# Optimization experiments

Measured on AMD Instinct MI355X. Metric: run time of the kernel, lower is better.

The kernel has to match this reference:

```python
import jax, jax.numpy as jnp
import numpy as np

T, H, I, E, SI, TOP_K = 1024, 2048, 1408, 60, 5632, 4


def setup_inputs() -> dict:
    key = jax.random.key(0)
    ks = jax.random.split(key, 9)
    s = 0.02  # typical init scale for weights
    return {
        "x": jax.random.normal(ks[0], (T, H), jnp.float32),
        "router_w": jax.random.normal(ks[1], (E, H), jnp.float32) * s,
        "w_gate": jax.random.normal(ks[2], (E, I, H), jnp.float32) * s,
        "w_up": jax.random.normal(ks[3], (E, I, H), jnp.float32) * s,
        "w_down": jax.random.normal(ks[4], (E, H, I), jnp.float32) * s,
        "sw_gate": jax.random.normal(ks[5], (SI, H), jnp.float32) * s,
        "sw_up": jax.random.normal(ks[6], (SI, H), jnp.float32) * s,
        "sw_down": jax.random.normal(ks[7], (H, SI), jnp.float32) * s,
        "shared_gate_w": jax.random.normal(ks[8], (1, H), jnp.float32) * s,
        "top_k": TOP_K,
    }


def reference(x, router_w, w_gate, w_up, w_down, sw_gate, sw_up, sw_down, shared_gate_w, top_k):
    Ttok, Hdim = x.shape
    Eexp = router_w.shape[0]
    # --- router: softmax over experts, top-k selection (norm_topk_prob=False) ---
    logits = x @ router_w.T                          # [T,E]
    probs = jax.nn.softmax(logits, axis=-1)
    topk_p, topk_i = jax.lax.top_k(probs, top_k)     # [T,k]
    # dense combine weights: zero for unrouted experts
    combine = jnp.zeros((Ttok, Eexp), x.dtype)
    combine = combine.at[jnp.arange(Ttok)[:, None], topk_i].set(topk_p)  # [T,E]

    # --- routed experts: SwiGLU MLP per expert, weighted accumulate (scan over E) ---
    def expert_step(acc, w):
        wg, wu, wd, c = w                            # [I,H],[I,H],[H,I],[T]
        h = jax.nn.silu(x @ wg.T) * (x @ wu.T)       # [T,I]
        return acc + c[:, None] * (h @ wd.T), None

    moe_out, _ = jax.lax.scan(expert_step, jnp.zeros_like(x),
                              (w_gate, w_up, w_down, combine.T))

    # --- shared expert with sigmoid gate ---
    shared = (jax.nn.silu(x @ sw_gate.T) * (x @ sw_up.T)) @ sw_down.T    # [T,H]
    shared = jax.nn.sigmoid(x @ shared_gate_w.T) * shared                # [T,1]*[T,H]
    return moe_out + shared
```

## Files before the change

### kernel.cpp

```cpp
#include <hip/hip_runtime.h>
#include <hip/hip_bf16.h>


typedef float  f32x4  __attribute__((ext_vector_type(4)));
typedef short  bf16x8 __attribute__((ext_vector_type(8)));
typedef unsigned short u16;
typedef unsigned int   u32;

constexpr int TT = 1024, HD = 2048, ID = 1408, NE = 60, SID = 5632, KTOP = 4;

#define GLDS(g, l) __builtin_amdgcn_global_load_lds( \
    (const __attribute__((address_space(1))) void*)(g), \
    (__attribute__((address_space(3))) void*)(l), 16, 0, 0)

__device__ __forceinline__ u16 f2bf(float f) {
    union { float f; u32 u; } v; v.f = f;
    u32 r = v.u + 0x7FFFu + ((v.u >> 16) & 1u);
    return (u16)(r >> 16);
}
__device__ __forceinline__ u32 cvtpk(float a, float b) {
    u32 r; asm("v_cvt_pk_bf16_f32 %0, %1, %2" : "=v"(r) : "v"(a), "v"(b));
    return r;
}
__device__ __forceinline__ bf16x8 fragF32(const float* tile, int r, int lk) {
    const float4* p = (const float4*)(tile + r * 32 + (((lk << 1) ^ ((r & 3) << 1)) << 2));
    float4 a = p[0], b = p[1];
    union { u32 u[4]; bf16x8 v; } rr;
    rr.u[0] = cvtpk(a.x, a.y); rr.u[1] = cvtpk(a.z, a.w);
    rr.u[2] = cvtpk(b.x, b.y); rr.u[3] = cvtpk(b.z, b.w);
    return rr.v;
}
__device__ __forceinline__ bf16x8 fragB16(const u16* tile, int r, int lk) {
    return *(const bf16x8*)(tile + r * 32 + ((lk ^ (r & 3)) << 3));
}

__global__ __launch_bounds__(64) void router_k(
    const float* __restrict__ x, const float* __restrict__ rw,
    const float* __restrict__ sgw,
    float* __restrict__ topk_p, int* __restrict__ topk_i,
    int* __restrict__ cnt, float* __restrict__ sgate)
{
    const int t = blockIdx.x, l = threadIdx.x;
    const float4* xr = ((const float4*)(x + (size_t)t * HD)) + l * 8;
    float4 xa[8];
    #pragma unroll
    for (int i = 0; i < 8; i++) xa[i] = xr[i];

    float le = 0.f;
    for (int e = 0; e < NE; e++) {
        const float4* wr = ((const float4*)(rw + (size_t)e * HD)) + l * 8;
        float a = 0.f;
        #pragma unroll
        for (int i = 0; i < 8; i++) {
            float4 wv = wr[i];
            a += xa[i].x * wv.x + xa[i].y * wv.y + xa[i].z * wv.z + xa[i].w * wv.w;
        }
        #pragma unroll
        for (int s = 32; s; s >>= 1) a += __shfl_xor(a, s);
        if (l == e) le = a;
    }
    {
        const float4* wr = ((const float4*)sgw) + l * 8;
        float a = 0.f;
        #pragma unroll
        for (int i = 0; i < 8; i++) {
            float4 wv = wr[i];
            a += xa[i].x * wv.x + xa[i].y * wv.y + xa[i].z * wv.z + xa[i].w * wv.w;
        }
        #pragma unroll
        for (int s = 32; s; s >>= 1) a += __shfl_xor(a, s);
        if (l == 0) sgate[t] = 1.f / (1.f + __expf(-a));
    }
    float mv = (l < NE) ? le : -3.4e38f;
    #pragma unroll
    for (int s = 32; s; s >>= 1) mv = fmaxf(mv, __shfl_xor(mv, s));
    float p = (l < NE) ? __expf(le - mv) : 0.f;
    float ss = p;
    #pragma unroll
    for (int s = 32; s; s >>= 1) ss += __shfl_xor(ss, s);
    p /= ss;
    float pv = (l < NE) ? p : -1.f;
    int   pi = l;
    float kp = 0.f; int ki = 0;
    for (int k = 0; k < KTOP; k++) {
        float bv = pv; int bi = pi;
        #pragma unroll
        for (int s = 32; s; s >>= 1) {
            float ov = __shfl_xor(bv, s); int oi = __shfl_xor(bi, s);
            if (ov > bv || (ov == bv && oi < bi)) { bv = ov; bi = oi; }
        }
        if (l == k) { kp = bv; ki = bi; }
        if (pi == bi) pv = -1.f;
    }
    if (l < KTOP) {
        topk_p[t * KTOP + l] = kp;
        topk_i[t * KTOP + l] = ki;
        atomicAdd(&cnt[ki], 1);
    }
}

__global__ __launch_bounds__(64) void prefix_k(const int* __restrict__ cnt, int* __restrict__ base)
{
    int l = threadIdx.x;
    if (l < NE) {
        int s = 0;
        for (int j = 0; j < l; j++) s += cnt[j];
        base[l] = s;
    }
}

__global__ __launch_bounds__(256) void scatter_k(
    const float* __restrict__ topk_p, const int* __restrict__ topk_i,
    const int* __restrict__ base, int* __restrict__ fill,
    int* __restrict__ slot_tok, float* __restrict__ slot_wt)
{
    int t = blockIdx.x * blockDim.x + threadIdx.x;
    if (t >= TT) return;
    for (int k = 0; k < KTOP; k++) {
        int e = topk_i[t * KTOP + k];
        int pos = atomicAdd(&fill[e], 1);
        int s = base[e] + pos;
        slot_tok[s] = t;
        slot_wt[s]  = topk_p[t * KTOP + k];
    }
}

template<bool GROUPED>
__global__ __launch_bounds__(256, 2) void gu_k(
    const float* __restrict__ X,
    const float* __restrict__ Wg, const float* __restrict__ Wu, size_t bStride,
    u16* __restrict__ H,
    const int* __restrict__ slot_tok, const float* __restrict__ slot_wt,
    const int* __restrict__ cnt, const int* __restrict__ basearr,
    int K, int N)
{
    __shared__ float Asl[2][128 * 32];
    __shared__ float Bgsl[2][64 * 32];
    __shared__ float Busl[2][64 * 32];
    const int tid = threadIdx.x, w = tid >> 6, lane = tid & 63;
    const int lm = lane & 15, lk = lane >> 4, wm0 = w * 32;
    const int e = GROUPED ? blockIdx.z : 0;
    const int mcnt = GROUPED ? cnt[e] : 128;
    const int mbase = GROUPED ? basearr[e] : blockIdx.y * 128;
    const float* Bg = Wg + (size_t)e * bStride + (size_t)blockIdx.x * 64 * K;
    const float* Bu = Wu + (size_t)e * bStride + (size_t)blockIdx.x * 64 * K;
    const int aofs = ((lane & 7) ^ (((lane >> 3) & 3) << 1)) << 2;
    const float* bgrow[2]; const float* burow[2];
    #pragma unroll
    for (int j = 0; j < 2; j++) {
        int rB = w * 16 + j * 8 + (lane >> 3);
        bgrow[j] = Bg + (size_t)rB * K + aofs;
        burow[j] = Bu + (size_t)rB * K + aofs;
    }
    const int nk = K >> 5;

    for (int mt = 0; GROUPED ? (mt * 128 < mcnt) : (mt == 0); ++mt) {
        const float* arow[4];
        #pragma unroll
        for (int j = 0; j < 4; j++) {
            int rA = w * 32 + j * 8 + (lane >> 3);
            int row;
            if constexpr (GROUPED) {
                int sl = mbase + mt * 128 + rA;
                row = (mt * 128 + rA < mcnt) ? slot_tok[sl] : 0;
            } else row = mbase + rA;
            arow[j] = X + (size_t)row * K + aofs;
        }
        f32x4 ag[2][4], au[2][4];
        #pragma unroll
        for (int mf = 0; mf < 2; mf++)
            #pragma unroll
            for (int nf = 0; nf < 4; nf++) {
                ag[mf][nf] = f32x4{0.f, 0.f, 0.f, 0.f};
                au[mf][nf] = f32x4{0.f, 0.f, 0.f, 0.f};
            }

        auto stage = [&](int b, int kt) {
            #pragma unroll
            for (int j = 0; j < 4; j++)
                GLDS(arow[j] + kt, &Asl[b][w * 1024 + j * 256]);
            #pragma unroll
            for (int j = 0; j < 2; j++) {
                GLDS(bgrow[j] + kt, &Bgsl[b][w * 512 + j * 256]);
                GLDS(burow[j] + kt, &Busl[b][w * 512 + j * 256]);
            }
        };

        stage(0, 0);
        __syncthreads();
        int cur = 0;
        for (int t = 0; t < nk; ++t) {
            if (t + 1 < nk) stage(cur ^ 1, (t + 1) << 5);
            const float* At  = &Asl[cur][0];
            const float* Bgt = &Bgsl[cur][0];
            const float* But = &Busl[cur][0];
            bf16x8 afr[2];
            #pragma unroll
            for (int mf = 0; mf < 2; mf++) afr[mf] = fragF32(At, wm0 + mf * 16 + lm, lk);
            #pragma unroll
            for (int nf = 0; nf < 4; nf++) {
                bf16x8 bgf = fragF32(Bgt, nf * 16 + lm, lk);
                bf16x8 buf_ = fragF32(But, nf * 16 + lm, lk);
                #pragma unroll
                for (int mf = 0; mf < 2; mf++) {
                    ag[mf][nf] = __builtin_amdgcn_mfma_f32_16x16x32_bf16(afr[mf], bgf, ag[mf][nf], 0, 0, 0);
                    au[mf][nf] = __builtin_amdgcn_mfma_f32_16x16x32_bf16(afr[mf], buf_, au[mf][nf], 0, 0, 0);
                }
            }
            __syncthreads();
            cur ^= 1;
        }

        #pragma unroll
        for (int mf = 0; mf < 2; mf++)
            #pragma unroll
            for (int j = 0; j < 4; j++) {
                int m = wm0 + mf * 16 + lk * 4 + j;
                bool valid = GROUPED ? (mt * 128 + m < mcnt) : true;
                if (valid) {
                    size_t row; float wt;
                    if constexpr (GROUPED) {
                        size_t sl = (size_t)(mbase + mt * 128 + m);
                        row = sl; wt = slot_wt[sl];
                    } else { row = (size_t)(mbase + m); wt = 1.f; }
                    #pragma unroll
                    for (int nf = 0; nf < 4; nf++) {
                        int col = blockIdx.x * 64 + nf * 16 + lm;
                        float g = ag[mf][nf][j], u = au[mf][nf][j];
                        float hv = g / (1.f + __expf(-g)) * u * wt;
                        H[row * (size_t)N + col] = f2bf(hv);
                    }
                }
            }
    }
}

template<bool GROUPED>
__global__ __launch_bounds__(256, 4) void down_k(
    const u16* __restrict__ Hb, const float* __restrict__ W0, size_t bStride,
    float* __restrict__ outF,
    const int* __restrict__ slot_tok, const float* __restrict__ sgate,
    const int* __restrict__ cnt, const int* __restrict__ basearr,
    int K, int kspan, int N)
{
    __shared__ u16   Asl[2][128 * 32];
    __shared__ float Bsl[2][64 * 32];
    const int tid = threadIdx.x, w = tid >> 6, lane = tid & 63;
    const int lm = lane & 15, lk = lane >> 4, wm0 = w * 32;
    const int e = GROUPED ? blockIdx.z : 0;
    const int mcnt = GROUPED ? cnt[e] : 128;
    const int mbase = GROUPED ? basearr[e] : blockIdx.y * 128;
    const int kbeg = GROUPED ? 0 : blockIdx.z * kspan;
    const int nk = (GROUPED ? K : kspan) >> 5;
    const float* Bp = W0 + (size_t)e * bStride + (size_t)blockIdx.x * 64 * K + kbeg;
    const int aofsF = ((lane & 7) ^ (((lane >> 3) & 3) << 1)) << 2;
    const int aofsH = ((lane & 3) ^ ((lane >> 2) & 3)) << 3;
    const float* brow[2];
    #pragma unroll
    for (int j = 0; j < 2; j++) {
        int rB = w * 16 + j * 8 + (lane >> 3);
        brow[j] = Bp + (size_t)rB * K + aofsF;
    }

    for (int mt = 0; GROUPED ? (mt * 128 < mcnt) : (mt == 0); ++mt) {
        const u16* arow[2];
        #pragma unroll
        for (int j = 0; j < 2; j++) {
            int rA = w * 32 + j * 16 + (lane >> 2);
            int row;
            if constexpr (GROUPED) {
                row = (mt * 128 + rA < mcnt) ? (mbase + mt * 128 + rA) : mbase;
            } else row = mbase + rA;
            arow[j] = Hb + (size_t)row * K + kbeg + aofsH;
        }
        f32x4 acc[2][4];
        #pragma unroll
        for (int mf = 0; mf < 2; mf++)
            #pragma unroll
            for (int nf = 0; nf < 4; nf++) acc[mf][nf] = f32x4{0.f, 0.f, 0.f, 0.f};

        auto stage = [&](int b, int kt) {
            #pragma unroll
            for (int j = 0; j < 2; j++)
                GLDS(arow[j] + kt, &Asl[b][w * 1024 + j * 512]);
            #pragma unroll
            for (int j = 0; j < 2; j++)
                GLDS(brow[j] + kt, &Bsl[b][w * 512 + j * 256]);
        };

        stage(0, 0);
        __syncthreads();
        int cur = 0;
        for (int t = 0; t < nk; ++t) {
            if (t + 1 < nk) stage(cur ^ 1, (t + 1) << 5);
            const u16*   At = &Asl[cur][0];
            const float* Bt = &Bsl[cur][0];
            bf16x8 afr[2];
            #pragma unroll
            for (int mf = 0; mf < 2; mf++) afr[mf] = fragB16(At, wm0 + mf * 16 + lm, lk);
            #pragma unroll
            for (int nf = 0; nf < 4; nf++) {
                bf16x8 bfr = fragF32(Bt, nf * 16 + lm, lk);
                #pragma unroll
                for (int mf = 0; mf < 2; mf++)
                    acc[mf][nf] = __builtin_amdgcn_mfma_f32_16x16x32_bf16(afr[mf], bfr, acc[mf][nf], 0, 0, 0);
            }
            __syncthreads();
            cur ^= 1;
        }

        #pragma unroll
        for (int mf = 0; mf < 2; mf++)
            #pragma unroll
            for (int j = 0; j < 4; j++) {
                int m = wm0 + mf * 16 + lk * 4 + j;
                bool valid = GROUPED ? (mt * 128 + m < mcnt) : true;
                if (valid) {
                    int tok; float scale;
                    if constexpr (GROUPED) {
                        tok = slot_tok[mbase + mt * 128 + m]; scale = 1.f;
                    } else { tok = mbase + m; scale = sgate[tok]; }
                    #pragma unroll
                    for (int nf = 0; nf < 4; nf++) {
                        int col = blockIdx.x * 64 + nf * 16 + lm;
                        atomicAdd(&outF[(size_t)tok * N + col], scale * acc[mf][nf][j]);
                    }
                }
            }
    }
}

extern "C" void kernel_launch(void* const* d_in, const int* in_sizes, int n_in,
                              void* d_out, int out_size, void* d_ws, size_t ws_size,
                              hipStream_t stream)
{
    const float* x      = (const float*)d_in[0];
    const float* rw     = (const float*)d_in[1];
    const float* w_gate = (const float*)d_in[2];
    const float* w_up   = (const float*)d_in[3];
    const float* w_down = (const float*)d_in[4];
    const float* sw_g   = (const float*)d_in[5];
    const float* sw_u   = (const float*)d_in[6];
    const float* sw_d   = (const float*)d_in[7];
    const float* sgw    = (const float*)d_in[8];
    float* out = (float*)d_out;

    char* ws = (char*)d_ws;
    int*   cnt      = (int*)(ws + 0);
    int*   fill     = (int*)(ws + 256);
    int*   basea    = (int*)(ws + 512);
    float* sgate    = (float*)(ws + 768);
    float* topk_p   = (float*)(ws + 5120);
    int*   topk_i   = (int*)(ws + 21504);
    int*   slot_tok = (int*)(ws + 37888);
    float* slot_wt  = (float*)(ws + 54272);
    u16*   h  = (u16*)(ws + 71680);
    u16*   hs = h + (size_t)4096 * ID;

    hipMemsetAsync(ws, 0, 512, stream);
    hipMemsetAsync(d_out, 0, (size_t)TT * HD * sizeof(float), stream);

    router_k<<<TT, 64, 0, stream>>>(x, rw, sgw, topk_p, topk_i, cnt, sgate);
    prefix_k<<<1, 64, 0, stream>>>(cnt, basea);
    scatter_k<<<4, 256, 0, stream>>>(topk_p, topk_i, basea, fill, slot_tok, slot_wt);

    gu_k<true><<<dim3(ID / 64, 1, NE), 256, 0, stream>>>(
        x, w_gate, w_up, (size_t)ID * HD, h,
        slot_tok, slot_wt, cnt, basea, HD, ID);
    gu_k<false><<<dim3(SID / 64, TT / 128, 1), 256, 0, stream>>>(
        x, sw_g, sw_u, 0, hs,
        nullptr, nullptr, nullptr, nullptr, HD, SID);
    down_k<true><<<dim3(HD / 64, 1, NE), 256, 0, stream>>>(
        h, w_down, (size_t)HD * ID, out,
        slot_tok, nullptr, cnt, basea, ID, 0, HD);
    down_k<false><<<dim3(HD / 64, TT / 128, 2), 256, 0, stream>>>(
        hs, sw_d, 0, out,
        nullptr, sgate, nullptr, nullptr, SID, SID / 2, HD);
}
```

Baseline: 831.9 us.

## Replace LDS-staged GEMMs with direct register-fragment loads and pre-converted bf16 activations

Drops the LDS double-buffered tiles in the gate/up and down GEMMs. Each wave now loads its MFMA fragments straight from global memory into registers with a two-stage software prefetch, over a 2x2 wave tile of 64x32. A new kernel converts x to bf16 once so activation fragments need no conversion in the inner loop. The shared down-projection now runs first without a K split and writes output directly, which removes the output memset and its atomics, and a small kernel replaces the counter memset. The trade is no LDS reuse across waves: each weight row is fetched by several waves and row reads are uncoalesced, with higher register pressure.

```diff
diff --git a/kernel.cpp b/kernel.cpp
--- a/kernel.cpp
+++ b/kernel.cpp
@@ -9,10 +9,6 @@
 
 constexpr int TT = 1024, HD = 2048, ID = 1408, NE = 60, SID = 5632, KTOP = 4;
 
-#define GLDS(g, l) __builtin_amdgcn_global_load_lds( \
-    (const __attribute__((address_space(1))) void*)(g), \
-    (__attribute__((address_space(3))) void*)(l), 16, 0, 0)
-
 __device__ __forceinline__ u16 f2bf(float f) {
     union { float f; u32 u; } v; v.f = f;
     u32 r = v.u + 0x7FFFu + ((v.u >> 16) & 1u);
@@ -22,16 +18,30 @@
     u32 r; asm("v_cvt_pk_bf16_f32 %0, %1, %2" : "=v"(r) : "v"(a), "v"(b));
     return r;
 }
-__device__ __forceinline__ bf16x8 fragF32(const float* tile, int r, int lk) {
-    const float4* p = (const float4*)(tile + r * 32 + (((lk << 1) ^ ((r & 3) << 1)) << 2));
-    float4 a = p[0], b = p[1];
+__device__ __forceinline__ bf16x8 cvt8(float4 a, float4 b) {
     union { u32 u[4]; bf16x8 v; } rr;
     rr.u[0] = cvtpk(a.x, a.y); rr.u[1] = cvtpk(a.z, a.w);
     rr.u[2] = cvtpk(b.x, b.y); rr.u[3] = cvtpk(b.z, b.w);
     return rr.v;
 }
-__device__ __forceinline__ bf16x8 fragB16(const u16* tile, int r, int lk) {
-    return *(const bf16x8*)(tile + r * 32 + ((lk ^ (r & 3)) << 3));
+__device__ __forceinline__ bf16x8 asbf(uint4 v) {
+    union { uint4 u; bf16x8 b; } c; c.u = v; return c.b;
+}
+
+__global__ void zero_k(int* __restrict__ p) { p[threadIdx.x] = 0; }
+
+__global__ __launch_bounds__(256) void xcvt_k(const float* __restrict__ x, u16* __restrict__ xb)
+{
+    size_t i = ((size_t)blockIdx.x * 256 + threadIdx.x) * 16;
+    const float4* p = (const float4*)(x + i);
+    float4 f0 = p[0], f1 = p[1], f2 = p[2], f3 = p[3];
+    uint4 o0, o1;
+    o0.x = cvtpk(f0.x, f0.y); o0.y = cvtpk(f0.z, f0.w);
+    o0.z = cvtpk(f1.x, f1.y); o0.w = cvtpk(f1.z, f1.w);
+    o1.x = cvtpk(f2.x, f2.y); o1.y = cvtpk(f2.z, f2.w);
+    o1.z = cvtpk(f3.x, f3.y); o1.w = cvtpk(f3.z, f3.w);
+    ((uint4*)(xb + i))[0] = o0;
+    ((uint4*)(xb + i))[1] = o1;
 }
 
 __global__ __launch_bounds__(64) void router_k(
@@ -127,92 +137,85 @@
 
 template<bool GROUPED>
 __global__ __launch_bounds__(256, 2) void gu_k(
-    const float* __restrict__ X,
+    const u16* __restrict__ Xb,
     const float* __restrict__ Wg, const float* __restrict__ Wu, size_t bStride,
     u16* __restrict__ H,
     const int* __restrict__ slot_tok, const float* __restrict__ slot_wt,
     const int* __restrict__ cnt, const int* __restrict__ basearr,
     int K, int N)
 {
-    __shared__ float Asl[2][128 * 32];
-    __shared__ float Bgsl[2][64 * 32];
-    __shared__ float Busl[2][64 * 32];
     const int tid = threadIdx.x, w = tid >> 6, lane = tid & 63;
-    const int lm = lane & 15, lk = lane >> 4, wm0 = w * 32;
+    const int lm = lane & 15, lk = lane >> 4;
+    const int wm0 = (w >> 1) * 64, wn0 = (w & 1) * 32;
     const int e = GROUPED ? blockIdx.z : 0;
     const int mcnt = GROUPED ? cnt[e] : 128;
-    const int mbase = GROUPED ? basearr[e] : blockIdx.y * 128;
-    const float* Bg = Wg + (size_t)e * bStride + (size_t)blockIdx.x * 64 * K;
-    const float* Bu = Wu + (size_t)e * bStride + (size_t)blockIdx.x * 64 * K;
-    const int aofs = ((lane & 7) ^ (((lane >> 3) & 3) << 1)) << 2;
-    const float* bgrow[2]; const float* burow[2];
-    #pragma unroll
-    for (int j = 0; j < 2; j++) {
-        int rB = w * 16 + j * 8 + (lane >> 3);
-        bgrow[j] = Bg + (size_t)rB * K + aofs;
-        burow[j] = Bu + (size_t)rB * K + aofs;
-    }
-    const int nk = K >> 5;
+    const int mbase = GROUPED ? basearr[e] : 0;
+
+    const float* gP[2]; const float* uP[2];
+    #pragma unroll
+    for (int nf = 0; nf < 2; nf++) {
+        size_t row = (size_t)(blockIdx.x * 64 + wn0 + nf * 16 + lm);
+        gP[nf] = Wg + (size_t)e * bStride + row * K + lk * 8;
+        uP[nf] = Wu + (size_t)e * bStride + row * K + lk * 8;
+    }
 
     for (int mt = 0; GROUPED ? (mt * 128 < mcnt) : (mt == 0); ++mt) {
-        const float* arow[4];
-        #pragma unroll
-        for (int j = 0; j < 4; j++) {
-            int rA = w * 32 + j * 8 + (lane >> 3);
+        const u16* aP[4];
+        #pragma unroll
+        for (int mf = 0; mf < 4; mf++) {
+            int mrow = wm0 + mf * 16 + lm;
             int row;
             if constexpr (GROUPED) {
-                int sl = mbase + mt * 128 + rA;
-                row = (mt * 128 + rA < mcnt) ? slot_tok[sl] : 0;
-            } else row = mbase + rA;
-            arow[j] = X + (size_t)row * K + aofs;
-        }
-        f32x4 ag[2][4], au[2][4];
-        #pragma unroll
-        for (int mf = 0; mf < 2; mf++)
+                int sl = mbase + mt * 128 + mrow;
+                row = (mt * 128 + mrow < mcnt) ? slot_tok[sl] : slot_tok[mbase];
+            } else row = blockIdx.y * 128 + mrow;
+            aP[mf] = Xb + (size_t)row * K + lk * 8;
+        }
+
+        f32x4 acc[2][4][2];
+        #pragma unroll
+        for (int m = 0; m < 2; m++)
             #pragma unroll
-            for (int nf = 0; nf < 4; nf++) {
-                ag[mf][nf] = f32x4{0.f, 0.f, 0.f, 0.f};
-                au[mf][nf] = f32x4{0.f, 0.f, 0.f, 0.f};
-            }
-
-        auto stage = [&](int b, int kt) {
-            #pragma unroll
-            for (int j = 0; j < 4; j++)
-                GLDS(arow[j] + kt, &Asl[b][w * 1024 + j * 256]);
-            #pragma unroll
-            for (int j = 0; j < 2; j++) {
-                GLDS(bgrow[j] + kt, &Bgsl[b][w * 512 + j * 256]);
-                GLDS(burow[j] + kt, &Busl[b][w * 512 + j * 256]);
-            }
-        };
-
-        stage(0, 0);
-        __syncthreads();
-        int cur = 0;
-        for (int t = 0; t < nk; ++t) {
-            if (t + 1 < nk) stage(cur ^ 1, (t + 1) << 5);
-            const float* At  = &Asl[cur][0];
-            const float* Bgt = &Bgsl[cur][0];
-            const float* But = &Busl[cur][0];
-            bf16x8 afr[2];
-            #pragma unroll
-            for (int mf = 0; mf < 2; mf++) afr[mf] = fragF32(At, wm0 + mf * 16 + lm, lk);
-            #pragma unroll
-            for (int nf = 0; nf < 4; nf++) {
-                bf16x8 bgf = fragF32(Bgt, nf * 16 + lm, lk);
-                bf16x8 buf_ = fragF32(But, nf * 16 + lm, lk);
+            for (int mf = 0; mf < 4; mf++)
                 #pragma unroll
-                for (int mf = 0; mf < 2; mf++) {
-                    ag[mf][nf] = __builtin_amdgcn_mfma_f32_16x16x32_bf16(afr[mf], bgf, ag[mf][nf], 0, 0, 0);
-                    au[mf][nf] = __builtin_amdgcn_mfma_f32_16x16x32_bf16(afr[mf], buf_, au[mf][nf], 0, 0, 0);
-                }
-            }
-            __syncthreads();
-            cur ^= 1;
-        }
-
-        #pragma unroll
-        for (int mf = 0; mf < 2; mf++)
+                for (int nf = 0; nf < 2; nf++)
+                    acc[m][mf][nf] = f32x4{0.f, 0.f, 0.f, 0.f};
+
+        uint4  a0[4], a1[4];
+        float4 g0[2][2], u0[2][2], g1[2][2], u1[2][2];
+
+#define LOADA(dst, kt) do { _Pragma("unroll") \
+        for (int mf = 0; mf < 4; mf++) dst[mf] = *(const uint4*)(aP[mf] + (kt)); } while (0)
+#define LOADB(dg, du, kt) do { _Pragma("unroll") \
+        for (int nf = 0; nf < 2; nf++) { \
+            const float4* pg = (const float4*)(gP[nf] + (kt)); \
+            dg[nf][0] = pg[0]; dg[nf][1] = pg[1]; \
+            const float4* pu = (const float4*)(uP[nf] + (kt)); \
+            du[nf][0] = pu[0]; du[nf][1] = pu[1]; } } while (0)
+#define COMPUTE(av, gv, uv) do { _Pragma("unroll") \
+        for (int nf = 0; nf < 2; nf++) { \
+            bf16x8 bg = cvt8(gv[nf][0], gv[nf][1]); \
+            bf16x8 bu = cvt8(uv[nf][0], uv[nf][1]); \
+            _Pragma("unroll") \
+            for (int mf = 0; mf < 4; mf++) { \
+                bf16x8 af = asbf(av[mf]); \
+                acc[0][mf][nf] = __builtin_amdgcn_mfma_f32_16x16x32_bf16(af, bg, acc[0][mf][nf], 0, 0, 0); \
+                acc[1][mf][nf] = __builtin_amdgcn_mfma_f32_16x16x32_bf16(af, bu, acc[1][mf][nf], 0, 0, 0); \
+            } } } while (0)
+
+        LOADA(a0, 0); LOADB(g0, u0, 0);
+        for (int kt = 0; kt < K; kt += 64) {
+            LOADA(a1, kt + 32); LOADB(g1, u1, kt + 32);
+            COMPUTE(a0, g0, u0);
+            if (kt + 64 < K) { LOADA(a0, kt + 64); LOADB(g0, u0, kt + 64); }
+            COMPUTE(a1, g1, u1);
+        }
+#undef LOADA
+#undef LOADB
+#undef COMPUTE
+
+        #pragma unroll
+        for (int mf = 0; mf < 4; mf++)
             #pragma unroll
             for (int j = 0; j < 4; j++) {
                 int m = wm0 + mf * 16 + lk * 4 + j;
@@ -222,11 +225,11 @@
                     if constexpr (GROUPED) {
                         size_t sl = (size_t)(mbase + mt * 128 + m);
                         row = sl; wt = slot_wt[sl];
-                    } else { row = (size_t)(mbase + m); wt = 1.f; }
+                    } else { row = (size_t)(blockIdx.y * 128 + m); wt = 1.f; }
                     #pragma unroll
-                    for (int nf = 0; nf < 4; nf++) {
-                        int col = blockIdx.x * 64 + nf * 16 + lm;
-                        float g = ag[mf][nf][j], u = au[mf][nf][j];
+                    for (int nf = 0; nf < 2; nf++) {
+                        int col = blockIdx.x * 64 + wn0 + nf * 16 + lm;
+                        float g = acc[0][mf][nf][j], u = acc[1][mf][nf][j];
                         float hv = g / (1.f + __expf(-g)) * u * wt;
                         H[row * (size_t)N + col] = f2bf(hv);
                     }
@@ -236,94 +239,92 @@
 }
 
 template<bool GROUPED>
-__global__ __launch_bounds__(256, 4) void down_k(
+__global__ __launch_bounds__(256, 3) void down_k(
     const u16* __restrict__ Hb, const float* __restrict__ W0, size_t bStride,
     float* __restrict__ outF,
     const int* __restrict__ slot_tok, const float* __restrict__ sgate,
     const int* __restrict__ cnt, const int* __restrict__ basearr,
-    int K, int kspan, int N)
-{
-    __shared__ u16   Asl[2][128 * 32];
-    __shared__ float Bsl[2][64 * 32];
+    int K, int N)
+{
     const int tid = threadIdx.x, w = tid >> 6, lane = tid & 63;
-    const int lm = lane & 15, lk = lane >> 4, wm0 = w * 32;
+    const int lm = lane & 15, lk = lane >> 4;
+    const int wm0 = (w >> 1) * 64, wn0 = (w & 1) * 32;
     const int e = GROUPED ? blockIdx.z : 0;
     const int mcnt = GROUPED ? cnt[e] : 128;
-    const int mbase = GROUPED ? basearr[e] : blockIdx.y * 128;
-    const int kbeg = GROUPED ? 0 : blockIdx.z * kspan;
-    const int nk = (GROUPED ? K : kspan) >> 5;
-    const float* Bp = W0 + (size_t)e * bStride + (size_t)blockIdx.x * 64 * K + kbeg;
-    const int aofsF = ((lane & 7) ^ (((lane >> 3) & 3) << 1)) << 2;
-    const int aofsH = ((lane & 3) ^ ((lane >> 2) & 3)) << 3;
-    const float* brow[2];
-    #pragma unroll
-    for (int j = 0; j < 2; j++) {
-        int rB = w * 16 + j * 8 + (lane >> 3);
-        brow[j] = Bp + (size_t)rB * K + aofsF;
+    const int mbase = GROUPED ? basearr[e] : 0;
+
+    const float* bP[2];
+    #pragma unroll
+    for (int nf = 0; nf < 2; nf++) {
+        size_t row = (size_t)(blockIdx.x * 64 + wn0 + nf * 16 + lm);
+        bP[nf] = W0 + (size_t)e * bStride + row * K + lk * 8;
     }
 
     for (int mt = 0; GROUPED ? (mt * 128 < mcnt) : (mt == 0); ++mt) {
-        const u16* arow[2];
-        #pragma unroll
-        for (int j = 0; j < 2; j++) {
-            int rA = w * 32 + j * 16 + (lane >> 2);
+        const u16* aP[4];
+        #pragma unroll
+        for (int mf = 0; mf < 4; mf++) {
+            int mrow = wm0 + mf * 16 + lm;
             int row;
             if constexpr (GROUPED) {
-                row = (mt * 128 + rA < mcnt) ? (mbase + mt * 128 + rA) : mbase;
-            } else row = mbase + rA;
-            arow[j] = Hb + (size_t)row * K + kbeg + aofsH;
-        }
-        f32x4 acc[2][4];
-        #pragma unroll
-        for (int mf = 0; mf < 2; mf++)
+                int sl = mbase + mt * 128 + mrow;
+                row = (mt * 128 + mrow < mcnt) ? sl : mbase;
+            } else row = blockIdx.y * 128 + mrow;
+            aP[mf] = Hb + (size_t)row * K + lk * 8;
+        }
+
+        f32x4 acc[4][2];
+        #pragma unroll
+        for (int mf = 0; mf < 4; mf++)
             #pragma unroll
-            for (int nf = 0; nf < 4; nf++) acc[mf][nf] = f32x4{0.f, 0.f, 0.f, 0.f};
-
-        auto stage = [&](int b, int kt) {
-            #pragma unroll
-            for (int j = 0; j < 2; j++)
-                GLDS(arow[j] + kt, &Asl[b][w * 1024 + j * 512]);
-            #pragma unroll
-            for (int j = 0; j < 2; j++)
-                GLDS(brow[j] + kt, &Bsl[b][w * 512 + j * 256]);
-        };
-
-        stage(0, 0);
-        __syncthreads();
-        int cur = 0;
-        for (int t = 0; t < nk; ++t) {
-            if (t + 1 < nk) stage(cur ^ 1, (t + 1) << 5);
-            const u16*   At = &Asl[cur][0];
-            const float* Bt = &Bsl[cur][0];
-            bf16x8 afr[2];
-            #pragma unroll
-            for (int mf = 0; mf < 2; mf++) afr[mf] = fragB16(At, wm0 + mf * 16 + lm, lk);
-            #pragma unroll
-            for (int nf = 0; nf < 4; nf++) {
-                bf16x8 bfr = fragF32(Bt, nf * 16 + lm, lk);
-                #pragma unroll
-                for (int mf = 0; mf < 2; mf++)
-                    acc[mf][nf] = __builtin_amdgcn_mfma_f32_16x16x32_bf16(afr[mf], bfr, acc[mf][nf], 0, 0, 0);
-            }
-            __syncthreads();
-            cur ^= 1;
-        }
-
-        #pragma unroll
-        for (int mf = 0; mf < 2; mf++)
+            for (int nf = 0; nf < 2; nf++)
+                acc[mf][nf] = f32x4{0.f, 0.f, 0.f, 0.f};
+
+        uint4  a0[4], a1[4];
+        float4 b0[2][2], b1[2][2];
+
+#define LOADA(dst, kt) do { _Pragma("unroll") \
+        for (int mf = 0; mf < 4; mf++) dst[mf] = *(const uint4*)(aP[mf] + (kt)); } while (0)
+#define LOADB(db, kt) do { _Pragma("unroll") \
+        for (int nf = 0; nf < 2; nf++) { \
+            const float4* pb = (const float4*)(bP[nf] + (kt)); \
+            db[nf][0] = pb[0]; db[nf][1] = pb[1]; } } while (0)
+#define COMPUTE(av, bv) do { _Pragma("unroll") \
+        for (int nf = 0; nf < 2; nf++) { \
+            bf16x8 bf_ = cvt8(bv[nf][0], bv[nf][1]); \
+            _Pragma("unroll") \
+            for (int mf = 0; mf < 4; mf++) \
+                acc[mf][nf] = __builtin_amdgcn_mfma_f32_16x16x32_bf16(asbf(av[mf]), bf_, acc[mf][nf], 0, 0, 0); \
+        } } while (0)
+
+        LOADA(a0, 0); LOADB(b0, 0);
+        for (int kt = 0; kt < K; kt += 64) {
+            LOADA(a1, kt + 32); LOADB(b1, kt + 32);
+            COMPUTE(a0, b0);
+            if (kt + 64 < K) { LOADA(a0, kt + 64); LOADB(b0, kt + 64); }
+            COMPUTE(a1, b1);
+        }
+#undef LOADA
+#undef LOADB
+#undef COMPUTE
+
+        #pragma unroll
+        for (int mf = 0; mf < 4; mf++)
             #pragma unroll
             for (int j = 0; j < 4; j++) {
                 int m = wm0 + mf * 16 + lk * 4 + j;
                 bool valid = GROUPED ? (mt * 128 + m < mcnt) : true;
                 if (valid) {
-                    int tok; float scale;
-                    if constexpr (GROUPED) {
-                        tok = slot_tok[mbase + mt * 128 + m]; scale = 1.f;
-                    } else { tok = mbase + m; scale = sgate[tok]; }
                     #pragma unroll
-                    for (int nf = 0; nf < 4; nf++) {
-                        int col = blockIdx.x * 64 + nf * 16 + lm;
-                        atomicAdd(&outF[(size_t)tok * N + col], scale * acc[mf][nf][j]);
+                    for (int nf = 0; nf < 2; nf++) {
+                        int col = blockIdx.x * 64 + wn0 + nf * 16 + lm;
+                        if constexpr (GROUPED) {
+                            int tok = slot_tok[mbase + mt * 128 + m];
+                            atomicAdd(&outF[(size_t)tok * N + col], acc[mf][nf][j]);
+                        } else {
+                            int tok = blockIdx.y * 128 + m;
+                            outF[(size_t)tok * N + col] = sgate[tok] * acc[mf][nf][j];
+                        }
                     }
                 }
             }
@@ -354,26 +355,26 @@
     int*   topk_i   = (int*)(ws + 21504);
     int*   slot_tok = (int*)(ws + 37888);
     float* slot_wt  = (float*)(ws + 54272);
-    u16*   h  = (u16*)(ws + 71680);
+    u16*   xb = (u16*)(ws + 71680);
+    u16*   h  = xb + (size_t)TT * HD;
     u16*   hs = h + (size_t)4096 * ID;
 
-    hipMemsetAsync(ws, 0, 512, stream);
-    hipMemsetAsync(d_out, 0, (size_t)TT * HD * sizeof(float), stream);
-
+    zero_k<<<1, 128, 0, stream>>>(cnt);
+    xcvt_k<<<512, 256, 0, stream>>>(x, xb);
     router_k<<<TT, 64, 0, stream>>>(x, rw, sgw, topk_p, topk_i, cnt, sgate);
     prefix_k<<<1, 64, 0, stream>>>(cnt, basea);
     scatter_k<<<4, 256, 0, stream>>>(topk_p, topk_i, basea, fill, slot_tok, slot_wt);
 
     gu_k<true><<<dim3(ID / 64, 1, NE), 256, 0, stream>>>(
-        x, w_gate, w_up, (size_t)ID * HD, h,
+        xb, w_gate, w_up, (size_t)ID * HD, h,
         slot_tok, slot_wt, cnt, basea, HD, ID);
     gu_k<false><<<dim3(SID / 64, TT / 128, 1), 256, 0, stream>>>(
-        x, sw_g, sw_u, 0, hs,
+        xb, sw_g, sw_u, 0, hs,
         nullptr, nullptr, nullptr, nullptr, HD, SID);
+    down_k<false><<<dim3(HD / 64, TT / 128, 1), 256, 0, stream>>>(
+        hs, sw_d, 0, out,
+        nullptr, sgate, nullptr, nullptr, SID, HD);
     down_k<true><<<dim3(HD / 64, 1, NE), 256, 0, stream>>>(
         h, w_down, (size_t)HD * ID, out,
-        slot_tok, nullptr, cnt, basea, ID, 0, HD);
-    down_k<false><<<dim3(HD / 64, TT / 128, 2), 256, 0, stream>>>(
-        hs, sw_d, 0, out,
-        nullptr, sgate, nullptr, nullptr, SID, SID / 2, HD);
-}
+        slot_tok, nullptr, cnt, basea, ID, HD);
+}
```

Result: slower. 1.341 ms (+61.1%).
